# Optimization experiments

Measured on AMD Instinct MI355X. Metric: run time of the kernel, lower is better.

Reference implementation:

```python
import jax, jax.numpy as jnp
import numpy as np

# Model config (matches init_kwargs)
D = 2048      # model dim
H = 16        # query heads
KVH = 4       # kv heads (GQA)
HD = 128      # head dim
G = H // KVH  # groups
CAP = 50.0    # soft cap (Gemma2-style)
EPS = 1e-6
SCALE = HD ** -0.5
B, T = 2, 2048


def _rmsnorm(x, gamma):
    # RMSNorm over last dim: x / sqrt(mean(x^2)+eps) * gamma
    return x * jax.lax.rsqrt(jnp.mean(x * x, axis=-1, keepdims=True) + EPS) * gamma


def setup_inputs() -> dict:
    key = jax.random.key(0)
    ks = jax.random.split(key, 5)
    s = 0.02
    return {
        "x": jax.random.normal(ks[0], (B, T, D), dtype=jnp.float32),
        "wq": jax.random.normal(ks[1], (H * HD, D), dtype=jnp.float32) * s,
        "wk": jax.random.normal(ks[2], (KVH * HD, D), dtype=jnp.float32) * s,
        "wv": jax.random.normal(ks[3], (KVH * HD, D), dtype=jnp.float32) * s,
        "wo": jax.random.normal(ks[4], (D, H * HD), dtype=jnp.float32) * s,
        "q_gamma": jnp.ones((HD,), dtype=jnp.float32),
        "k_gamma": jnp.ones((HD,), dtype=jnp.float32),
    }


def reference(x, wq, wk, wv, wo, q_gamma, k_gamma):
    b, t, _ = x.shape
    # Projections (nn.Linear: x @ W^T), split into heads -> (b, h, t, hd)
    q = (x @ wq.T).reshape(b, t, H, HD).transpose(0, 2, 1, 3)
    k = (x @ wk.T).reshape(b, t, KVH, HD).transpose(0, 2, 1, 3)
    v = (x @ wv.T).reshape(b, t, KVH, HD).transpose(0, 2, 1, 3)
    # QK-norm (per-head-dim RMSNorm)
    q = _rmsnorm(q, q_gamma)
    k = _rmsnorm(k, k_gamma)
    # GQA: expand kv heads to match query heads (repeat_interleave on head axis)
    k = jnp.repeat(k, G, axis=1)
    v = jnp.repeat(v, G, axis=1)
    # Scores with tanh soft-cap, causal mask, softmax
    attn = jnp.einsum('bhtd,bhsd->bhts', q, k) * SCALE
    attn = CAP * jnp.tanh(attn / CAP)
    causal = jnp.triu(jnp.ones((t, t), dtype=bool), k=1)
    attn = jnp.where(causal, -jnp.inf, attn)
    attn = jax.nn.softmax(attn, axis=-1)
    out = jnp.einsum('bhts,bhsd->bhtd', attn, v)
    out = out.transpose(0, 2, 1, 3).reshape(b, t, H * HD)
    return out @ wo.T
```

## Files before the change

### kernel.cpp

```cpp
#include <hip/hip_runtime.h>

typedef __attribute__((ext_vector_type(4))) float f32x4;
typedef __attribute__((ext_vector_type(8))) short bf16x8;
typedef __attribute__((ext_vector_type(4))) unsigned short us4;
typedef unsigned short ushort_t;

__device__ __forceinline__ float bf2f(ushort_t u){
  union { unsigned int i; float f; } v; v.i = ((unsigned int)u) << 16; return v.f;
}
__device__ __forceinline__ ushort_t f2bf(float f){
  union { float f; unsigned int i; } v; v.f = f;
  unsigned int r = v.i + 0x7fffu + ((v.i >> 16) & 1u);
  return (ushort_t)(r >> 16);
}
__device__ __forceinline__ void async16(const ushort_t* g, ushort_t* l){
  __builtin_amdgcn_global_load_lds(
      (const __attribute__((address_space(1))) unsigned int*)g,
      (__attribute__((address_space(3))) unsigned int*)l, 16, 0, 0);
}

__global__ void detect_f32(const ushort_t* __restrict__ probe, int* __restrict__ flag){
  const int lane = threadIdx.x;
  int big = 0;
  for (int i = lane; i < 4096; i += 64) {
    const int ex = (probe[i] >> 7) & 0xFF;
    if (ex >= 0x90) big++;
  }
#pragma unroll
  for (int off = 32; off > 0; off >>= 1) big += __shfl_xor(big, off);
  if (lane == 0) *flag = (big > 16) ? 1 : 0;
}

__global__ __launch_bounds__(256) void convert_all(
    const void* s0, const void* s1, const void* s2, const void* s3,
    const void* s4, const void* s5, const void* s6,
    ushort_t* d0, ushort_t* d1, ushort_t* d2, ushort_t* d3,
    ushort_t* d4, ushort_t* d5, ushort_t* d6,
    const int* __restrict__ flag)
{
  long i = ((long)blockIdx.x * 256 + threadIdx.x) * 4;
  if (i >= 18874624L) return;
  const void* src; ushort_t* dst; long loc;
  if      (i <  8388608L) { src = s0; dst = d0; loc = i; }
  else if (i < 12582912L) { src = s1; dst = d1; loc = i - 8388608L; }
  else if (i < 13631488L) { src = s2; dst = d2; loc = i - 12582912L; }
  else if (i < 14680064L) { src = s3; dst = d3; loc = i - 13631488L; }
  else if (i < 18874368L) { src = s4; dst = d4; loc = i - 14680064L; }
  else if (i < 18874496L) { src = s5; dst = d5; loc = i - 18874368L; }
  else                    { src = s6; dst = d6; loc = i - 18874496L; }
  if (*flag != 0) {
    f32x4 v = *(const f32x4*)((const float*)src + loc);
    us4 o; o[0] = f2bf(v[0]); o[1] = f2bf(v[1]); o[2] = f2bf(v[2]); o[3] = f2bf(v[3]);
    *(us4*)(dst + loc) = o;
  } else {
    *(us4*)(dst + loc) = *(const us4*)((const ushort_t*)src + loc);
  }
}

#define BK 64
__global__ __launch_bounds__(256) void qkv_gemm(
    const ushort_t* __restrict__ A,
    const ushort_t* __restrict__ Wq, const ushort_t* __restrict__ Wk,
    const ushort_t* __restrict__ Wv,
    ushort_t* __restrict__ Q, ushort_t* __restrict__ Kb, ushort_t* __restrict__ Vt)
{
  __shared__ __align__(16) ushort_t As[128*BK];
  __shared__ __align__(16) ushort_t Bs[128*BK];
  const int tid = threadIdx.x;
  const int lane = tid & 63, wave = tid >> 6;
  const int quad = lane >> 4, l16 = lane & 15;
  const int m0 = blockIdx.y * 128;
  const int n0g = blockIdx.x * 128;
  const ushort_t* B; int n0, mode;
  if      (n0g < 2048) { B = Wq; n0 = n0g;        mode = 0; }
  else if (n0g < 2560) { B = Wk; n0 = n0g - 2048; mode = 1; }
  else                 { B = Wv; n0 = n0g - 2560; mode = 2; }
  const int wm = (wave >> 1) * 64, wn = (wave & 1) * 64;
  const int srow = lane >> 3, sslot = lane & 7;

  f32x4 acc[4][4];
#pragma unroll
  for (int i = 0; i < 4; i++)
#pragma unroll
    for (int j = 0; j < 4; j++) acc[i][j] = (f32x4){0.f,0.f,0.f,0.f};

  for (int k0 = 0; k0 < 2048; k0 += BK) {
    __syncthreads();
#pragma unroll
    for (int i = 0; i < 4; i++) {
      const int r0 = wave*32 + i*8;
      const int row = r0 + srow;
      const int g = (sslot ^ (row & 7)) * 8;
      async16(A + (size_t)(m0 + row)*2048 + k0 + g, &As[r0*64]);
      async16(B + (size_t)(n0 + row)*2048 + k0 + g, &Bs[r0*64]);
    }
    __syncthreads();
#pragma unroll
    for (int kc = 0; kc < 2; kc++) {
      bf16x8 af[4], bfr[4];
#pragma unroll
      for (int i = 0; i < 4; i++) {
        const int ra = wm + i*16 + l16;
        af[i] = *(const bf16x8*)&As[ra*64 + (((kc*4 + quad) ^ (ra & 7)))*8];
        const int rb = wn + i*16 + l16;
        bfr[i] = *(const bf16x8*)&Bs[rb*64 + (((kc*4 + quad) ^ (rb & 7)))*8];
      }
#pragma unroll
      for (int i = 0; i < 4; i++)
#pragma unroll
        for (int j = 0; j < 4; j++)
          acc[i][j] = __builtin_amdgcn_mfma_f32_16x16x32_bf16(af[i], bfr[j], acc[i][j], 0, 0, 0);
    }
  }
#pragma unroll
  for (int i = 0; i < 4; i++) {
    const int rbase = m0 + wm + i*16 + quad*4;
#pragma unroll
    for (int j = 0; j < 4; j++) {
      const int col = n0 + wn + j*16 + l16;
      if (mode == 0) {
#pragma unroll
        for (int r = 0; r < 4; r++) Q[(size_t)(rbase + r)*2048 + col] = f2bf(acc[i][j][r]);
      } else if (mode == 1) {
#pragma unroll
        for (int r = 0; r < 4; r++) Kb[(size_t)(rbase + r)*512 + col] = f2bf(acc[i][j][r]);
      } else {
        us4 pk;
#pragma unroll
        for (int r = 0; r < 4; r++) pk[r] = f2bf(acc[i][j][r]);
        const size_t addr = (size_t)((rbase >> 11)*512 + col)*2048 + (rbase & 2047);
        *(us4*)&Vt[addr] = pk;
      }
    }
  }
}

__global__ __launch_bounds__(256) void rmsnorm_rows(
    ushort_t* __restrict__ buf, const ushort_t* __restrict__ gamma)
{
  const int lane = threadIdx.x & 63, wave = threadIdx.x >> 6;
  const int quad = lane >> 4, l16 = lane & 15;
  const int vec = blockIdx.x*16 + wave*4 + quad;
  const size_t base = (size_t)vec*128 + l16*8;
  bf16x8 v = *(const bf16x8*)&buf[base];
  float f[8]; float ss = 0.f;
#pragma unroll
  for (int j = 0; j < 8; j++) { f[j] = bf2f((ushort_t)v[j]); ss += f[j]*f[j]; }
#pragma unroll
  for (int off = 1; off < 16; off <<= 1) ss += __shfl_xor(ss, off);
  const float sc = rsqrtf(ss * (1.0f/128.0f) + 1e-6f);
  bf16x8 g = *(const bf16x8*)&gamma[l16*8];
  bf16x8 o;
#pragma unroll
  for (int j = 0; j < 8; j++) o[j] = (short)f2bf(f[j]*sc*bf2f((ushort_t)g[j]));
  *(bf16x8*)&buf[base] = o;
}

__global__ __launch_bounds__(256, 3) void attn_fused(
    const ushort_t* __restrict__ qbuf, const ushort_t* __restrict__ kbuf,
    const ushort_t* __restrict__ vtbuf, const ushort_t* __restrict__ qgamma,
    ushort_t* __restrict__ obuf)
{
  __shared__ __align__(16) ushort_t Ks[64*128];
  __shared__ __align__(16) ushort_t VTs[128*64];
  __shared__ __align__(16) ushort_t Ps[4][16*72];
  const int tid = threadIdx.x;
  const int lane = tid & 63, wave = tid >> 6;
  const int quad = lane >> 4, l16 = lane & 15;
  const int bx = 31 - blockIdx.x;
  const int h = blockIdx.y, b = blockIdx.z;
  const int kvh = h >> 2;
  const size_t bT = (size_t)b * 2048;
  const int qrow = bx*64 + wave*16 + l16;
  const size_t vbase = ((size_t)(b*4 + kvh)) * 128 * 2048;

  const ushort_t* qptr = qbuf + (bT + qrow)*2048 + h*128;
  float qv[4][8];
  float ss = 0.f;
#pragma unroll
  for (int kc = 0; kc < 4; kc++) {
    bf16x8 v = *(const bf16x8*)&qptr[kc*32 + quad*8];
#pragma unroll
    for (int j = 0; j < 8; j++) { float f = bf2f((ushort_t)v[j]); qv[kc][j] = f; ss += f*f; }
  }
  ss += __shfl_xor(ss, 16);
  ss += __shfl_xor(ss, 32);
  const float qsc = rsqrtf(ss*(1.0f/128.0f) + 1e-6f) * 0.08838834764831845f;
  bf16x8 qf[4];
#pragma unroll
  for (int kc = 0; kc < 4; kc++) {
    bf16x8 g = *(const bf16x8*)&qgamma[kc*32 + quad*8];
    bf16x8 o;
#pragma unroll
    for (int j = 0; j < 8; j++) o[j] = (short)f2bf(qv[kc][j] * qsc * bf2f((ushort_t)g[j]));
    qf[kc] = o;
  }

  f32x4 Ob[8];
#pragma unroll
  for (int i = 0; i < 8; i++) Ob[i] = (f32x4){0.f,0.f,0.f,0.f};
  float l_run = 0.f;

  const ushort_t* kg0 = kbuf + (bT + wave*16 + (lane>>4))*512 + kvh*128;
  const ushort_t* vg0 = vtbuf + vbase + (size_t)(wave*32 + (lane>>3))*2048;
  bf16x8 kreg[4], vreg[4];
  auto loadKV = [&](int kb){
#pragma unroll
    for (int i = 0; i < 4; i++) {
      const int sw = ((lane & 15) ^ ((i*4 + (lane>>4)) & 15)) * 8;
      kreg[i] = *(const bf16x8*)(kg0 + (size_t)(kb*64 + i*4)*512 + sw);
    }
#pragma unroll
    for (int i = 0; i < 4; i++) {
      const int sw = ((lane & 7) ^ ((i*8 + (lane>>3)) & 7)) * 8;
      vreg[i] = *(const bf16x8*)(vg0 + (size_t)(i*8)*2048 + kb*64 + sw);
    }
  };
  auto writeKV = [&](){
#pragma unroll
    for (int i = 0; i < 4; i++)
      *(bf16x8*)&Ks[(wave*16 + i*4)*128 + lane*8] = kreg[i];
#pragma unroll
    for (int i = 0; i < 4; i++)
      *(bf16x8*)&VTs[(wave*32 + i*8)*64 + lane*8] = vreg[i];
  };

  loadKV(0);
  writeKV();
  __syncthreads();

  for (int kb = 0; kb <= bx; kb++) {
    const bool last = (kb == bx);
    if (!last) loadKV(kb+1);

    f32x4 st[4];
#pragma unroll
    for (int s = 0; s < 4; s++) {
      f32x4 c = (f32x4){0.f,0.f,0.f,0.f};
#pragma unroll
      for (int kc = 0; kc < 4; kc++) {
        const int row = s*16 + l16;
        const bf16x8 kf = *(const bf16x8*)&Ks[row*128 + (((kc*4 + quad) ^ (row & 15)))*8];
        c = __builtin_amdgcn_mfma_f32_16x16x32_bf16(kf, qf[kc], c, 0, 0, 0);
      }
      st[s] = c;
    }

    const int myq = wave*16 + l16;
    float rsum = 0.f;
#pragma unroll
    for (int s = 0; s < 4; s++) {
      us4 pk;
#pragma unroll
      for (int r = 0; r < 4; r++) {
        const float x = st[s][r];
        const float w = x*x;
        const float t2 = x * __builtin_fmaf(w,
            __builtin_fmaf(w, 3.0777494e-8f, -1.9235934e-4f), 1.4426950408889634f);
        float p = __builtin_amdgcn_exp2f(t2);
        if (last && (s*16 + quad*4 + r) > myq) p = 0.f;
        rsum += p;
        pk[r] = f2bf(p);
      }
      *(us4*)&Ps[wave][l16*72 + s*16 + quad*4] = pk;
    }
    l_run += rsum;

#pragma unroll
    for (int kc = 0; kc < 2; kc++) {
      const bf16x8 pf = *(const bf16x8*)&Ps[wave][l16*72 + kc*32 + quad*8];
#pragma unroll
      for (int dt = 0; dt < 8; dt++) {
        const int d = dt*16 + l16;
        const bf16x8 vf = *(const bf16x8*)&VTs[d*64 + (((kc*4 + quad) ^ (d & 7)))*8];
        Ob[dt] = __builtin_amdgcn_mfma_f32_16x16x32_bf16(vf, pf, Ob[dt], 0, 0, 0);
      }
    }

    if (!last) {
      __builtin_amdgcn_s_waitcnt(0xC07F);
      __builtin_amdgcn_s_barrier();
      writeKV();
      __syncthreads();
    }
  }

  l_run += __shfl_xor(l_run, 16);
  l_run += __shfl_xor(l_run, 32);
  const float inv_l = __builtin_amdgcn_rcpf(l_run);
  ushort_t* optr = obuf + (bT + qrow)*2048 + h*128;
#pragma unroll
  for (int dt = 0; dt < 8; dt++) {
    us4 pk;
#pragma unroll
    for (int r = 0; r < 4; r++) pk[r] = f2bf(Ob[dt][r] * inv_l);
    *(us4*)&optr[dt*16 + quad*4] = pk;
  }
}

__global__ __launch_bounds__(256) void gemm_final(
    const ushort_t* __restrict__ A, const ushort_t* __restrict__ B,
    ushort_t* __restrict__ C, float* __restrict__ Cf, const int* __restrict__ flag)
{
  __shared__ __align__(16) ushort_t As[128*BK];
  __shared__ __align__(16) ushort_t Bs[128*BK];
  const int tid = threadIdx.x;
  const int lane = tid & 63, wave = tid >> 6;
  const int quad = lane >> 4, l16 = lane & 15;
  const int m0 = blockIdx.y * 128, n0 = blockIdx.x * 128;
  const int wm = (wave >> 1) * 64, wn = (wave & 1) * 64;
  const int srow = lane >> 3, sslot = lane & 7;

  f32x4 acc[4][4];
#pragma unroll
  for (int i = 0; i < 4; i++)
#pragma unroll
    for (int j = 0; j < 4; j++) acc[i][j] = (f32x4){0.f,0.f,0.f,0.f};

  for (int k0 = 0; k0 < 2048; k0 += BK) {
    __syncthreads();
#pragma unroll
    for (int i = 0; i < 4; i++) {
      const int r0 = wave*32 + i*8;
      const int row = r0 + srow;
      const int g = (sslot ^ (row & 7)) * 8;
      async16(A + (size_t)(m0 + row)*2048 + k0 + g, &As[r0*64]);
      async16(B + (size_t)(n0 + row)*2048 + k0 + g, &Bs[r0*64]);
    }
    __syncthreads();
#pragma unroll
    for (int kc = 0; kc < 2; kc++) {
      bf16x8 af[4], bfr[4];
#pragma unroll
      for (int i = 0; i < 4; i++) {
        const int ra = wm + i*16 + l16;
        af[i] = *(const bf16x8*)&As[ra*64 + (((kc*4 + quad) ^ (ra & 7)))*8];
        const int rb = wn + i*16 + l16;
        bfr[i] = *(const bf16x8*)&Bs[rb*64 + (((kc*4 + quad) ^ (rb & 7)))*8];
      }
#pragma unroll
      for (int i = 0; i < 4; i++)
#pragma unroll
        for (int j = 0; j < 4; j++)
          acc[i][j] = __builtin_amdgcn_mfma_f32_16x16x32_bf16(af[i], bfr[j], acc[i][j], 0, 0, 0);
    }
  }
  const bool isf = (*flag != 0);
#pragma unroll
  for (int i = 0; i < 4; i++) {
    const int rbase = m0 + wm + i*16 + quad*4;
#pragma unroll
    for (int j = 0; j < 4; j++) {
      const int col = n0 + wn + j*16 + l16;
#pragma unroll
      for (int r = 0; r < 4; r++) {
        if (isf) Cf[(size_t)(rbase + r)*2048 + col] = acc[i][j][r];
        else     C [(size_t)(rbase + r)*2048 + col] = f2bf(acc[i][j][r]);
      }
    }
  }
}

extern "C" void kernel_launch(void* const* d_in, const int* in_sizes, int n_in,
                              void* d_out, int out_size, void* d_ws, size_t ws_size,
                              hipStream_t stream)
{
  int* flag = (int*)d_ws;
  ushort_t* ws = (ushort_t*)d_ws + 8;
  ushort_t* xb  = ws;
  ushort_t* wqb = xb  + (size_t)8388608;
  ushort_t* wkb = wqb + (size_t)4194304;
  ushort_t* wvb = wkb + (size_t)1048576;
  ushort_t* wob = wvb + (size_t)1048576;
  ushort_t* qgb = wob + (size_t)4194304;
  ushort_t* kgb = qgb + 128;
  ushort_t* qbuf = kgb + 128;
  ushort_t* kbuf  = qbuf + (size_t)8388608;
  ushort_t* vtbuf = kbuf + (size_t)2097152;
  ushort_t* obuf = xb;

  detect_f32<<<1, 64, 0, stream>>>((const ushort_t*)d_in[1], flag);
  convert_all<<<18433, 256, 0, stream>>>(
      d_in[0], d_in[1], d_in[2], d_in[3], d_in[4], d_in[5], d_in[6],
      xb, wqb, wkb, wvb, wob, qgb, kgb, flag);

  qkv_gemm<<<dim3(24, 32), 256, 0, stream>>>(xb, wqb, wkb, wvb, qbuf, kbuf, vtbuf);
  rmsnorm_rows<<<dim3(1024), 256, 0, stream>>>(kbuf, kgb);
  attn_fused<<<dim3(32, 16, 2), 256, 0, stream>>>(qbuf, kbuf, vtbuf, qgb, obuf);
  gemm_final<<<dim3(16, 32), 256, 0, stream>>>(obuf, wob, (ushort_t*)d_out, (float*)d_out, flag);
}
```

Before: 391.3 us.

## Process two 64-row query tiles per attention block to reuse K/V tiles

```diff
diff --git a/kernel.cpp b/kernel.cpp
--- a/kernel.cpp
+++ b/kernel.cpp
@@ -156,50 +156,67 @@
   *(bf16x8*)&buf[base] = o;
 }
 
-__global__ __launch_bounds__(256, 3) void attn_fused(
+__global__ __launch_bounds__(256, 2) void attn_fused(
     const ushort_t* __restrict__ qbuf, const ushort_t* __restrict__ kbuf,
     const ushort_t* __restrict__ vtbuf, const ushort_t* __restrict__ qgamma,
     ushort_t* __restrict__ obuf)
 {
   __shared__ __align__(16) ushort_t Ks[64*128];
   __shared__ __align__(16) ushort_t VTs[128*64];
-  __shared__ __align__(16) ushort_t Ps[4][16*72];
+  __shared__ __align__(16) ushort_t Ps[4][2][16*72];
   const int tid = threadIdx.x;
   const int lane = tid & 63, wave = tid >> 6;
   const int quad = lane >> 4, l16 = lane & 15;
-  const int bx = 31 - blockIdx.x;
+  const int bx = 15 - blockIdx.x;
   const int h = blockIdx.y, b = blockIdx.z;
   const int kvh = h >> 2;
   const size_t bT = (size_t)b * 2048;
-  const int qrow = bx*64 + wave*16 + l16;
+  const int qrow0 = bx*128 + wave*16 + l16;
+  const int qrow1 = qrow0 + 64;
   const size_t vbase = ((size_t)(b*4 + kvh)) * 128 * 2048;
-
-  const ushort_t* qptr = qbuf + (bT + qrow)*2048 + h*128;
-  float qv[4][8];
-  float ss = 0.f;
-#pragma unroll
-  for (int kc = 0; kc < 4; kc++) {
-    bf16x8 v = *(const bf16x8*)&qptr[kc*32 + quad*8];
-#pragma unroll
-    for (int j = 0; j < 8; j++) { float f = bf2f((ushort_t)v[j]); qv[kc][j] = f; ss += f*f; }
-  }
-  ss += __shfl_xor(ss, 16);
-  ss += __shfl_xor(ss, 32);
-  const float qsc = rsqrtf(ss*(1.0f/128.0f) + 1e-6f) * 0.08838834764831845f;
-  bf16x8 qf[4];
-#pragma unroll
-  for (int kc = 0; kc < 4; kc++) {
-    bf16x8 g = *(const bf16x8*)&qgamma[kc*32 + quad*8];
-    bf16x8 o;
-#pragma unroll
-    for (int j = 0; j < 8; j++) o[j] = (short)f2bf(qv[kc][j] * qsc * bf2f((ushort_t)g[j]));
-    qf[kc] = o;
-  }
-
-  f32x4 Ob[8];
-#pragma unroll
-  for (int i = 0; i < 8; i++) Ob[i] = (f32x4){0.f,0.f,0.f,0.f};
-  float l_run = 0.f;
+  const int myq = wave*16 + l16;
+
+  bf16x8 qf0[4], qf1[4];
+  {
+    const ushort_t* qp0 = qbuf + (bT + qrow0)*2048 + h*128;
+    const ushort_t* qp1 = qbuf + (bT + qrow1)*2048 + h*128;
+    float qv0[4][8], qv1[4][8];
+    float ss0 = 0.f, ss1 = 0.f;
+#pragma unroll
+    for (int kc = 0; kc < 4; kc++) {
+      bf16x8 v0 = *(const bf16x8*)&qp0[kc*32 + quad*8];
+      bf16x8 v1 = *(const bf16x8*)&qp1[kc*32 + quad*8];
+#pragma unroll
+      for (int j = 0; j < 8; j++) {
+        float f0 = bf2f((ushort_t)v0[j]); qv0[kc][j] = f0; ss0 += f0*f0;
+        float f1 = bf2f((ushort_t)v1[j]); qv1[kc][j] = f1; ss1 += f1*f1;
+      }
+    }
+    ss0 += __shfl_xor(ss0, 16); ss0 += __shfl_xor(ss0, 32);
+    ss1 += __shfl_xor(ss1, 16); ss1 += __shfl_xor(ss1, 32);
+    const float sc0 = rsqrtf(ss0*(1.0f/128.0f) + 1e-6f) * 0.08838834764831845f;
+    const float sc1 = rsqrtf(ss1*(1.0f/128.0f) + 1e-6f) * 0.08838834764831845f;
+#pragma unroll
+    for (int kc = 0; kc < 4; kc++) {
+      bf16x8 g = *(const bf16x8*)&qgamma[kc*32 + quad*8];
+      bf16x8 o0, o1;
+#pragma unroll
+      for (int j = 0; j < 8; j++) {
+        const float gg = bf2f((ushort_t)g[j]);
+        o0[j] = (short)f2bf(qv0[kc][j] * sc0 * gg);
+        o1[j] = (short)f2bf(qv1[kc][j] * sc1 * gg);
+      }
+      qf0[kc] = o0; qf1[kc] = o1;
+    }
+  }
+
+  f32x4 Ob0[8], Ob1[8];
+#pragma unroll
+  for (int i = 0; i < 8; i++) { Ob0[i] = (f32x4){0.f,0.f,0.f,0.f}; Ob1[i] = (f32x4){0.f,0.f,0.f,0.f}; }
+  float l0 = 0.f, l1 = 0.f;
+
+  ushort_t* ps0 = &Ps[wave][0][l16*72];
+  ushort_t* ps1 = &Ps[wave][1][l16*72];
 
   const ushort_t* kg0 = kbuf + (bT + wave*16 + (lane>>4))*512 + kvh*128;
   const ushort_t* vg0 = vtbuf + vbase + (size_t)(wave*32 + (lane>>3))*2048;
@@ -225,76 +242,117 @@
       *(bf16x8*)&VTs[(wave*32 + i*8)*64 + lane*8] = vreg[i];
   };
 
-  loadKV(0);
-  writeKV();
-  __syncthreads();
-
-  for (int kb = 0; kb <= bx; kb++) {
-    const bool last = (kb == bx);
-    if (!last) loadKV(kb+1);
-
-    f32x4 st[4];
+  auto sm = [&](f32x4* st, ushort_t* psb, bool diag) -> float {
+    float rsum = 0.f;
 #pragma unroll
     for (int s = 0; s < 4; s++) {
-      f32x4 c = (f32x4){0.f,0.f,0.f,0.f};
-#pragma unroll
-      for (int kc = 0; kc < 4; kc++) {
-        const int row = s*16 + l16;
-        const bf16x8 kf = *(const bf16x8*)&Ks[row*128 + (((kc*4 + quad) ^ (row & 15)))*8];
-        c = __builtin_amdgcn_mfma_f32_16x16x32_bf16(kf, qf[kc], c, 0, 0, 0);
-      }
-      st[s] = c;
-    }
-
-    const int myq = wave*16 + l16;
-    float rsum = 0.f;
-#pragma unroll
-    for (int s = 0; s < 4; s++) {
-      us4 pk;
+      float p[4];
 #pragma unroll
       for (int r = 0; r < 4; r++) {
         const float x = st[s][r];
         const float w = x*x;
         const float t2 = x * __builtin_fmaf(w,
             __builtin_fmaf(w, 3.0777494e-8f, -1.9235934e-4f), 1.4426950408889634f);
-        float p = __builtin_amdgcn_exp2f(t2);
-        if (last && (s*16 + quad*4 + r) > myq) p = 0.f;
-        rsum += p;
-        pk[r] = f2bf(p);
-      }
-      *(us4*)&Ps[wave][l16*72 + s*16 + quad*4] = pk;
-    }
-    l_run += rsum;
+        float pp = __builtin_amdgcn_exp2f(t2);
+        if (diag && (s*16 + quad*4 + r) > myq) pp = 0.f;
+        rsum += pp;
+        p[r] = pp;
+      }
+      uint2 pk;
+      pk.x = (__float_as_uint(p[0]) >> 16) | (__float_as_uint(p[1]) & 0xFFFF0000u);
+      pk.y = (__float_as_uint(p[2]) >> 16) | (__float_as_uint(p[3]) & 0xFFFF0000u);
+      *(uint2*)&psb[s*16 + quad*4] = pk;
+    }
+    return rsum;
+  };
+
+  loadKV(0);
+  writeKV();
+  __syncthreads();
+
+  const int ndiag = 2*bx;
+  for (int kb = 0; kb <= ndiag; kb++) {
+    loadKV(kb+1);
+
+    f32x4 st0[4], st1[4];
+#pragma unroll
+    for (int s = 0; s < 4; s++) { st0[s] = (f32x4){0.f,0.f,0.f,0.f}; st1[s] = (f32x4){0.f,0.f,0.f,0.f}; }
+#pragma unroll
+    for (int s = 0; s < 4; s++) {
+      const int row = s*16 + l16;
+#pragma unroll
+      for (int kc = 0; kc < 4; kc++) {
+        const bf16x8 kf = *(const bf16x8*)&Ks[row*128 + (((kc*4 + quad) ^ (row & 15)))*8];
+        st0[s] = __builtin_amdgcn_mfma_f32_16x16x32_bf16(kf, qf0[kc], st0[s], 0, 0, 0);
+        st1[s] = __builtin_amdgcn_mfma_f32_16x16x32_bf16(kf, qf1[kc], st1[s], 0, 0, 0);
+      }
+    }
+
+    if (kb == ndiag) l0 += sm(st0, ps0, true);
+    else             l0 += sm(st0, ps0, false);
+    l1 += sm(st1, ps1, false);
 
 #pragma unroll
     for (int kc = 0; kc < 2; kc++) {
-      const bf16x8 pf = *(const bf16x8*)&Ps[wave][l16*72 + kc*32 + quad*8];
+      const bf16x8 pf0 = *(const bf16x8*)&ps0[kc*32 + quad*8];
+      const bf16x8 pf1 = *(const bf16x8*)&ps1[kc*32 + quad*8];
 #pragma unroll
       for (int dt = 0; dt < 8; dt++) {
         const int d = dt*16 + l16;
         const bf16x8 vf = *(const bf16x8*)&VTs[d*64 + (((kc*4 + quad) ^ (d & 7)))*8];
-        Ob[dt] = __builtin_amdgcn_mfma_f32_16x16x32_bf16(vf, pf, Ob[dt], 0, 0, 0);
-      }
-    }
-
-    if (!last) {
-      __builtin_amdgcn_s_waitcnt(0xC07F);
-      __builtin_amdgcn_s_barrier();
-      writeKV();
-      __syncthreads();
-    }
-  }
-
-  l_run += __shfl_xor(l_run, 16);
-  l_run += __shfl_xor(l_run, 32);
-  const float inv_l = __builtin_amdgcn_rcpf(l_run);
-  ushort_t* optr = obuf + (bT + qrow)*2048 + h*128;
+        Ob0[dt] = __builtin_amdgcn_mfma_f32_16x16x32_bf16(vf, pf0, Ob0[dt], 0, 0, 0);
+        Ob1[dt] = __builtin_amdgcn_mfma_f32_16x16x32_bf16(vf, pf1, Ob1[dt], 0, 0, 0);
+      }
+    }
+
+    __builtin_amdgcn_s_waitcnt(0xC07F);
+    __builtin_amdgcn_s_barrier();
+    writeKV();
+    __syncthreads();
+  }
+
+  {
+    f32x4 st1[4];
+#pragma unroll
+    for (int s = 0; s < 4; s++) st1[s] = (f32x4){0.f,0.f,0.f,0.f};
+#pragma unroll
+    for (int s = 0; s < 4; s++) {
+      const int row = s*16 + l16;
+#pragma unroll
+      for (int kc = 0; kc < 4; kc++) {
+        const bf16x8 kf = *(const bf16x8*)&Ks[row*128 + (((kc*4 + quad) ^ (row & 15)))*8];
+        st1[s] = __builtin_amdgcn_mfma_f32_16x16x32_bf16(kf, qf1[kc], st1[s], 0, 0, 0);
+      }
+    }
+    l1 += sm(st1, ps1, true);
+#pragma unroll
+    for (int kc = 0; kc < 2; kc++) {
+      const bf16x8 pf1 = *(const bf16x8*)&ps1[kc*32 + quad*8];
+#pragma unroll
+      for (int dt = 0; dt < 8; dt++) {
+        const int d = dt*16 + l16;
+        const bf16x8 vf = *(const bf16x8*)&VTs[d*64 + (((kc*4 + quad) ^ (d & 7)))*8];
+        Ob1[dt] = __builtin_amdgcn_mfma_f32_16x16x32_bf16(vf, pf1, Ob1[dt], 0, 0, 0);
+      }
+    }
+  }
+
+  l0 += __shfl_xor(l0, 16); l0 += __shfl_xor(l0, 32);
+  l1 += __shfl_xor(l1, 16); l1 += __shfl_xor(l1, 32);
+  const float inv0 = __builtin_amdgcn_rcpf(l0);
+  const float inv1 = __builtin_amdgcn_rcpf(l1);
+  ushort_t* op0 = obuf + (bT + qrow0)*2048 + h*128;
+  ushort_t* op1 = obuf + (bT + qrow1)*2048 + h*128;
 #pragma unroll
   for (int dt = 0; dt < 8; dt++) {
-    us4 pk;
-#pragma unroll
-    for (int r = 0; r < 4; r++) pk[r] = f2bf(Ob[dt][r] * inv_l);
-    *(us4*)&optr[dt*16 + quad*4] = pk;
+    us4 pk0, pk1;
+#pragma unroll
+    for (int r = 0; r < 4; r++) {
+      pk0[r] = f2bf(Ob0[dt][r] * inv0);
+      pk1[r] = f2bf(Ob1[dt][r] * inv1);
+    }
+    *(us4*)&op0[dt*16 + quad*4] = pk0;
+    *(us4*)&op1[dt*16 + quad*4] = pk1;
   }
 }
 
@@ -386,6 +444,6 @@
 
   qkv_gemm<<<dim3(24, 32), 256, 0, stream>>>(xb, wqb, wkb, wvb, qbuf, kbuf, vtbuf);
   rmsnorm_rows<<<dim3(1024), 256, 0, stream>>>(kbuf, kgb);
-  attn_fused<<<dim3(32, 16, 2), 256, 0, stream>>>(qbuf, kbuf, vtbuf, qgb, obuf);
+  attn_fused<<<dim3(16, 16, 2), 256, 0, stream>>>(qbuf, kbuf, vtbuf, qgb, obuf);
   gemm_final<<<dim3(16, 32), 256, 0, stream>>>(obuf, wob, (ushort_t*)d_out, (float*)d_out, flag);
 }
```

After: 341.2 us. 12.8% less time.
